# Optimization experiments

Hardware: AMD Instinct MI355X
Metric: run time of the kernel (lower is better)

The kernel has to match this reference:

```python
import jax, jax.numpy as jnp
import numpy as np

B, H, DK, DV = 64, 32, 128, 128


def setup_inputs() -> dict:
    key = jax.random.key(0)
    ks = jax.random.split(key, 6)
    return {
        "S": jax.random.normal(ks[0], (B, H, DK, DV), dtype=jnp.float32),
        "k": jax.random.normal(ks[1], (B, H, DK), dtype=jnp.float32),
        "v": jax.random.normal(ks[2], (B, H, DV), dtype=jnp.float32),
        "q": jax.random.normal(ks[3], (B, H, DK), dtype=jnp.float32),
        "alpha": jax.random.uniform(ks[4], (B, H, DK), dtype=jnp.float32),
        "beta": jax.random.uniform(ks[5], (B, H, 1), dtype=jnp.float32),
    }


def reference(S, k, v, q, alpha, beta):
    # S_t = (I - beta k k^T) Diag(alpha) S_{t-1} + beta k v^T ;  o_t = S_t^T q
    S_decay = alpha[..., None] * S                              # (B,H,dk,dv)
    kT_S = jnp.einsum('bhd,bhdv->bhv', k, S_decay)              # k^T (Diag(a) S)
    kkT_S = k[..., :, None] * kT_S[..., None, :]                # outer(k, k^T S)
    kvT = k[..., :, None] * v[..., None, :]                     # outer(k, v)
    S_new = S_decay - beta[..., None] * kkT_S + beta[..., None] * kvT
    o = jnp.einsum('bhdv,bhd->bhv', S_new, q)
    return (S_new, o)
```

## Files before the change

### kernel.cpp

```cpp
#include <hip/hip_runtime.h>


#define DK 128
#define DV 128

__global__ __launch_bounds__(128) void kda_update_kernel(
    const float* __restrict__ S,
    const float* __restrict__ k,
    const float* __restrict__ v,
    const float* __restrict__ q,
    const float* __restrict__ alpha,
    const float* __restrict__ beta,
    float* __restrict__ Sout,
    float* __restrict__ o)
{
    const int bh = blockIdx.x;
    const int e  = threadIdx.x;

    __shared__ float sak[DK];
    __shared__ float sa[DK];
    __shared__ float sk[DK];
    __shared__ float sq[DK];

    const size_t hoff = (size_t)bh * DK * DV;
    const float* __restrict__ Sbh = S + hoff;

    {
        const float kk = k[(size_t)bh * DK + e];
        const float aa = alpha[(size_t)bh * DK + e];
        sk[e]  = kk;
        sa[e]  = aa;
        sak[e] = kk * aa;
        sq[e]  = q[(size_t)bh * DK + e];
    }
    __syncthreads();

    float s_col[DK];
    float kts = 0.f;
    #pragma unroll
    for (int d = 0; d < DK; ++d) {
        s_col[d] = Sbh[(size_t)d * DV + e];
        kts += sak[d] * s_col[d];
    }

    const float coef = beta[bh] * (v[(size_t)bh * DV + e] - kts);

    float oacc = 0.f;
    float* __restrict__ Sobh = Sout + hoff;
    #pragma unroll
    for (int d = 0; d < DK; ++d) {
        const float sn = sa[d] * s_col[d] + sk[d] * coef;
        __builtin_nontemporal_store(sn, Sobh + (size_t)d * DV + e);
        oacc += sq[d] * sn;
    }

    o[(size_t)bh * DV + e] = oacc;
}

extern "C" void kernel_launch(void* const* d_in, const int* in_sizes, int n_in,
                              void* d_out, int out_size, void* d_ws, size_t ws_size,
                              hipStream_t stream) {
    const float* S     = (const float*)d_in[0];
    const float* k     = (const float*)d_in[1];
    const float* v     = (const float*)d_in[2];
    const float* q     = (const float*)d_in[3];
    const float* alpha = (const float*)d_in[4];
    const float* beta  = (const float*)d_in[5];

    const int BH = in_sizes[5];

    float* Sout = (float*)d_out;
    float* o    = Sout + (size_t)BH * DK * DV;

    kda_update_kernel<<<dim3(BH), dim3(128), 0, stream>>>(S, k, v, q, alpha, beta, Sout, o);
}
```

Baseline: 44.47 us.

## Vectorize S access to float4, one wave per head, re-read S instead of caching

Each 64-lane wave now handles one (b,h) head, four heads per 256-thread block. Each lane owns four contiguous columns and half of the DK rows, loading and storing S as float4 instead of scalars. Partial sums from the two row halves are combined with a cross-half shuffle. The 128-register column cache is dropped, so S is read twice (once for k^T S, once for the update). The intent is wider memory transactions and lower register pressure, at the cost of doubled S read traffic, which may partly hit in cache.

```diff
diff --git a/kernel.cpp b/kernel.cpp
--- a/kernel.cpp
+++ b/kernel.cpp
@@ -4,7 +4,9 @@
 #define DK 128
 #define DV 128
 
-__global__ __launch_bounds__(128) void kda_update_kernel(
+typedef float v4f __attribute__((ext_vector_type(4)));
+
+__global__ __launch_bounds__(256) void kda_update_kernel(
     const float* __restrict__ S,
     const float* __restrict__ k,
     const float* __restrict__ v,
@@ -14,47 +16,64 @@
     float* __restrict__ Sout,
     float* __restrict__ o)
 {
-    const int bh = blockIdx.x;
-    const int e  = threadIdx.x;
+    const int wave  = threadIdx.x >> 6;
+    const int lane  = threadIdx.x & 63;
+    const int bh    = blockIdx.x * 4 + wave;
+    const int e0    = (lane & 31) * 4;
+    const int dbase = (lane >> 5) * 64;
 
-    __shared__ float sak[DK];
-    __shared__ float sa[DK];
-    __shared__ float sk[DK];
-    __shared__ float sq[DK];
+    __shared__ float sak[4][DK];
+    __shared__ float sa[4][DK];
+    __shared__ float sk[4][DK];
+    __shared__ float sq[4][DK];
+
+    for (int i = lane; i < DK; i += 64) {
+        const float kk = k[(size_t)bh * DK + i];
+        const float aa = alpha[(size_t)bh * DK + i];
+        sk[wave][i]  = kk;
+        sa[wave][i]  = aa;
+        sak[wave][i] = kk * aa;
+        sq[wave][i]  = q[(size_t)bh * DK + i];
+    }
+    __syncthreads();
 
     const size_t hoff = (size_t)bh * DK * DV;
     const float* __restrict__ Sbh = S + hoff;
 
-    {
-        const float kk = k[(size_t)bh * DK + e];
-        const float aa = alpha[(size_t)bh * DK + e];
-        sk[e]  = kk;
-        sa[e]  = aa;
-        sak[e] = kk * aa;
-        sq[e]  = q[(size_t)bh * DK + e];
+    v4f kts = {0.f, 0.f, 0.f, 0.f};
+    #pragma unroll 16
+    for (int i = 0; i < 64; ++i) {
+        const int d = dbase + i;
+        const v4f sv = *reinterpret_cast<const v4f*>(Sbh + (size_t)d * DV + e0);
+        kts += sak[wave][d] * sv;
     }
-    __syncthreads();
+    kts.x += __shfl_xor(kts.x, 32);
+    kts.y += __shfl_xor(kts.y, 32);
+    kts.z += __shfl_xor(kts.z, 32);
+    kts.w += __shfl_xor(kts.w, 32);
 
-    float s_col[DK];
-    float kts = 0.f;
-    #pragma unroll
-    for (int d = 0; d < DK; ++d) {
-        s_col[d] = Sbh[(size_t)d * DV + e];
-        kts += sak[d] * s_col[d];
+    const float b  = beta[bh];
+    const v4f  vv  = *reinterpret_cast<const v4f*>(v + (size_t)bh * DV + e0);
+    const v4f  coef = b * (vv - kts);
+
+    v4f oacc = {0.f, 0.f, 0.f, 0.f};
+    float* __restrict__ Sobh = Sout + hoff;
+    #pragma unroll 16
+    for (int i = 0; i < 64; ++i) {
+        const int d = dbase + i;
+        const v4f sv = *reinterpret_cast<const v4f*>(Sbh + (size_t)d * DV + e0);
+        const v4f sn = sa[wave][d] * sv + sk[wave][d] * coef;
+        __builtin_nontemporal_store(sn, reinterpret_cast<v4f*>(Sobh + (size_t)d * DV + e0));
+        oacc += sq[wave][d] * sn;
     }
+    oacc.x += __shfl_xor(oacc.x, 32);
+    oacc.y += __shfl_xor(oacc.y, 32);
+    oacc.z += __shfl_xor(oacc.z, 32);
+    oacc.w += __shfl_xor(oacc.w, 32);
 
-    const float coef = beta[bh] * (v[(size_t)bh * DV + e] - kts);
-
-    float oacc = 0.f;
-    float* __restrict__ Sobh = Sout + hoff;
-    #pragma unroll
-    for (int d = 0; d < DK; ++d) {
-        const float sn = sa[d] * s_col[d] + sk[d] * coef;
-        __builtin_nontemporal_store(sn, Sobh + (size_t)d * DV + e);
-        oacc += sq[d] * sn;
+    if (lane < 32) {
+        *reinterpret_cast<v4f*>(o + (size_t)bh * DV + e0) = oacc;
     }
-
-    o[(size_t)bh * DV + e] = oacc;
 }
 
 extern "C" void kernel_launch(void* const* d_in, const int* in_sizes, int n_in,
@@ -72,5 +91,5 @@
     float* Sout = (float*)d_out;
     float* o    = Sout + (size_t)BH * DK * DV;
 
-    kda_update_kernel<<<dim3(BH), dim3(128), 0, stream>>>(S, k, v, q, alpha, beta, Sout, o);
+    kda_update_kernel<<<dim3(BH / 4), dim3(256), 0, stream>>>(S, k, v, q, alpha, beta, Sout, o);
 }
```

Result: slower. 67.91 us (+52.7%).
